# Kernel optimization log

Measured on AMD Instinct MI355X. Metric: run time of the kernel, lower is better.

## Reference

```python
import jax, jax.numpy as jnp
import numpy as np

JITTER = 0.1

def se_kernel(X, X2, length_scale):
    # K[i,j] = exp(-||x_i - x2_j||^2 / length_scale^2)   (no 1/2 factor, as in source)
    Xs = X / length_scale
    X2s = X2 / length_scale
    d2 = (jnp.sum(Xs * Xs, axis=1)[:, None]
          - 2.0 * Xs @ X2s.T
          + jnp.sum(X2s * X2s, axis=1)[None, :])
    return jnp.exp(-d2)

def kron(A, B):
    # kronecker(A, B) as in source: einsum 'ab,cd->acbd' then reshape
    return jnp.einsum('ab,cd->acbd', A, B).reshape(A.shape[0] * B.shape[0], A.shape[1] * B.shape[1])

def setup_inputs() -> dict:
    key = jax.random.key(0)
    ks = jax.random.split(key, 5)
    return {
        'space_coordinates': jax.random.normal(ks[0], (150, 3), dtype=jnp.float32),
        'time_coordinates': jax.random.normal(ks[1], (40, 1), dtype=jnp.float32),
        'stData': jax.random.normal(ks[2], (150, 40), dtype=jnp.float32),
        'test_space_coordinates': jax.random.normal(ks[3], (200, 3), dtype=jnp.float32),
        'test_time_coordinates': jax.random.normal(ks[4], (30, 1), dtype=jnp.float32),
        'log_latlong_length_scale': jnp.log(jnp.asarray(1.0, dtype=jnp.float32)),
        'log_elevation_length_scale': jnp.log(jnp.asarray(1.0, dtype=jnp.float32)),
        'log_time_length_scale': jnp.log(jnp.asarray(0.25, dtype=jnp.float32)),
        'log_noise_variance': jnp.log(jnp.asarray(0.1, dtype=jnp.float32)),
        'log_signal_variance': jnp.log(jnp.asarray(1.0, dtype=jnp.float32)),
    }

def reference(space_coordinates, time_coordinates, stData,
              test_space_coordinates, test_time_coordinates,
              log_latlong_length_scale, log_elevation_length_scale,
              log_time_length_scale, log_noise_variance, log_signal_variance):
    ll = jnp.exp(log_latlong_length_scale)
    le = jnp.exp(log_elevation_length_scale)
    lt = jnp.exp(log_time_length_scale)
    Ns = space_coordinates.shape[0]
    Nt = time_coordinates.shape[0]

    # ---- update(): build sigma_inverse and alpha via Kronecker eigendecomposition ----
    spatial_K = (se_kernel(space_coordinates[:, 0:2], space_coordinates[:, 0:2], ll)
                 * se_kernel(space_coordinates[:, 2:3], space_coordinates[:, 2:3], le)
                 + JITTER * jnp.eye(Ns, dtype=space_coordinates.dtype))
    temporal_K = (se_kernel(time_coordinates, time_coordinates, lt)
                  + JITTER * jnp.eye(Nt, dtype=time_coordinates.dtype))
    ws, Vs = jnp.linalg.eigh(spatial_K)
    wt, Vt = jnp.linalg.eigh(temporal_K)
    V = kron(Vt, Vs)                                   # [N, N], N = Nt*Ns
    w = jnp.einsum('a,b->ab', wt, ws).reshape(-1)      # eigenvalues of kron kernel
    inv = 1.0 / (w + jnp.exp(log_noise_variance))
    sigma_inverse = (V * inv[None, :]) @ V.T           # V diag(inv) V^T
    alpha = sigma_inverse @ stData.T.reshape(-1, 1)    # [N, 1]

    # ---- forward ----
    test_spatial = (se_kernel(test_space_coordinates[:, 0:2], space_coordinates[:, 0:2], ll)
                    * se_kernel(test_space_coordinates[:, 2:3], space_coordinates[:, 2:3], le))
    test_temporal = se_kernel(test_time_coordinates, time_coordinates, lt)
    Kst = kron(test_temporal, test_spatial)            # [M, N], M = Mt*Ms
    yPred = Kst @ alpha                                # [M, 1]
    # fused row-wise quadratic form: diag(Kst sigma_inverse Kst^T)
    yVar = jnp.exp(log_signal_variance) - jnp.sum((Kst @ sigma_inverse) * Kst, axis=1)
    Mt = test_time_coordinates.shape[0]
    Ms = test_space_coordinates.shape[0]
    yPred = yPred.reshape(Mt, Ms).T                    # [Ms, Mt]
    yVar = yVar.reshape(Mt, Ms).T                      # [Ms, Mt]
    return (yPred, yVar)
```

## Files before the change

kernel.cpp:

```cpp
#include <hip/hip_runtime.h>
#include <math.h>

#define NS 150
#define LDW 152
#define NPACK 11848
#define NT 40
#define MS 200
#define MT 30
#define N_SWEEPS 6
#define ROUNDS (N_SWEEPS*(NT-1))
#define JITTER 0.1f
#define NTHR 512

#define OFF_MP    0
#define OFF_PR    47392
#define OFF_INVS  52256
#define OFF_DVS   52288
#define OFF_SCS   52896
#define OFF_TSCS  54704
#define OFF_QV    57104
#define OFF_RV    57904
#define OFF_GV    58704
#define OFF_ACOL  59304
#define OFF_WTJ   59424
#define SMEM_BYTES 59440
#define OFF_A2    0
#define OFF_VTS   13120
#define OFF_PRM   20160
#define OFF_TCS   22720

__device__ __forceinline__ int rs_off(int r) {
    int g = r >> 2, rm = r & 3;
    return LDW * r - 8 * g * (g - 1) - 4 * rm * g;
}

__device__ __forceinline__ void jac_params(const float (*A)[NT+1], float4* dst,
                                           int i, int rr) {
    int i0 = i, i1 = NT - 1 - i;
    int p = (i0 == 0) ? 0 : ((i0 - 1 + rr) % (NT - 1)) + 1;
    int q = ((i1 - 1 + rr) % (NT - 1)) + 1;
    if (p > q) { int tsw = p; p = q; q = tsw; }
    float app = A[p][p], aqq = A[q][q], apq = A[p][q];
    float c, s;
    if (apq == 0.0f) { c = 1.0f; s = 0.0f; }
    else {
        float tau = (aqq - app) / (2.0f * apq);
        float tt = ((tau >= 0.0f) ? 1.0f : -1.0f) / (fabsf(tau) + sqrtf(1.0f + tau*tau));
        c = rsqrtf(1.0f + tt*tt);
        s = tt * c;
    }
    dst[i] = make_float4(c, s, __int_as_float(p), __int_as_float(q));
}

__global__ void __launch_bounds__(NTHR, 2) gp_block(
        const float* __restrict__ sc,  const float* __restrict__ tc,
        const float* __restrict__ st,  const float* __restrict__ tsc,
        const float* __restrict__ ttc,
        const float* __restrict__ lll, const float* __restrict__ lle,
        const float* __restrict__ llt, const float* __restrict__ lnv,
        const float* __restrict__ lsv, float* __restrict__ out) {
    __shared__ __align__(16) char smem[SMEM_BYTES];
    int j = blockIdx.x, tid = threadIdx.x;

    auto A2   = (float (*)[NT][NT+1])(smem + OFF_A2);
    auto Vts  = (float (*)[44])(smem + OFF_VTS);
    auto prm  = (float4 (*)[NT/2])(smem + OFF_PRM);
    float* tcs  = (float*)(smem + OFF_TCS);
    float* gv   = (float*)(smem + OFF_GV);
    float* Acol = (float*)(smem + OFF_ACOL);
    float* wtjs = (float*)(smem + OFF_WTJ);
    float* scs  = (float*)(smem + OFF_SCS);
    float* tscs = (float*)(smem + OFF_TSCS);

    float ilt2 = expf(-2.0f * llt[0]);
    if (tid < NT) tcs[tid] = tc[tid];
    for (int t = tid; t < NS*3; t += NTHR) scs[t] = sc[t];
    for (int t = tid; t < MS*3; t += NTHR) tscs[t] = tsc[t];
    __syncthreads();
    for (int idx = tid; idx < NT*NT; idx += NTHR) {
        int i = idx / NT, jj = idx - i*NT;
        float dt = tcs[i] - tcs[jj];
        float v = expf(-dt*dt*ilt2);
        if (i == jj) v += JITTER;
        A2[0][i][jj] = v;
    }
    for (int idx = tid; idx < NT*44; idx += NTHR) {
        int jr = idx / 44, k = idx - jr*44;
        Vts[jr][k] = (jr == k) ? 1.0f : 0.0f;
    }
    __syncthreads();
    int wave = tid >> 6, lane = tid & 63;
    for (int rd = 0; rd < ROUNDS; ++rd) {
        int cur = rd & 1, nxt = cur ^ 1;
        float4* wp = prm[wave];
        if (lane < NT/2) jac_params(A2[cur], wp, lane, rd % (NT - 1));
        __builtin_amdgcn_wave_barrier();
        for (int t = tid; t < 600; t += NTHR) {
            if (t < 400) {
                int bi = t / 20, bj = t - bi*20;
                float4 Pi = wp[bi], Pj = wp[bj];
                int pi = __float_as_int(Pi.z), qi = __float_as_int(Pi.w);
                int pj = __float_as_int(Pj.z), qj = __float_as_int(Pj.w);
                float ci = Pi.x, si = Pi.y, cj = Pj.x, sj = Pj.y;
                float a00 = A2[cur][pi][pj], a01 = A2[cur][pi][qj];
                float a10 = A2[cur][qi][pj], a11 = A2[cur][qi][qj];
                float b00 = ci*a00 - si*a10, b01 = ci*a01 - si*a11;
                float b10 = si*a00 + ci*a10, b11 = si*a01 + ci*a11;
                A2[nxt][pi][pj] = cj*b00 - sj*b01; A2[nxt][pi][qj] = sj*b00 + cj*b01;
                A2[nxt][qi][pj] = cj*b10 - sj*b11; A2[nxt][qi][qj] = sj*b10 + cj*b11;
            } else {
                int u2 = t - 400;
                int pr = u2 / 10, ch = (u2 - pr*10) << 2;
                float4 P = wp[pr];
                int pj = __float_as_int(P.z), qj = __float_as_int(P.w);
                float c = P.x, s = P.y;
                float4 vp = *(float4*)&Vts[pj][ch];
                float4 vq = *(float4*)&Vts[qj][ch];
                float4 np, nq;
                np.x = c*vp.x - s*vq.x; nq.x = s*vp.x + c*vq.x;
                np.y = c*vp.y - s*vq.y; nq.y = s*vp.y + c*vq.y;
                np.z = c*vp.z - s*vq.z; nq.z = s*vp.z + c*vq.z;
                np.w = c*vp.w - s*vq.w; nq.w = s*vp.w + c*vq.w;
                *(float4*)&Vts[pj][ch] = np;
                *(float4*)&Vts[qj][ch] = nq;
            }
        }
        __syncthreads();
    }
    const int fin = ROUNDS & 1;
    if (tid == 0) wtjs[0] = A2[fin][j][j];
    for (int s = tid; s < NS; s += NTHR) {
        const float4* va = (const float4*)&Vts[j][0];
        const float4* sa = (const float4*)&st[s*NT];
        float acc = 0.0f;
        #pragma unroll
        for (int c4 = 0; c4 < NT/4; ++c4) {
            float4 a = va[c4], b = sa[c4];
            acc += a.x*b.x + a.y*b.y + a.z*b.z + a.w*b.w;
        }
        gv[s] = acc;
    }
    if (tid < MT) {
        float ttv = ttc[tid];
        float acc = 0.0f;
        for (int t = 0; t < NT; ++t) {
            float dt = ttv - tcs[t];
            acc += expf(-dt*dt*ilt2) * Vts[j][t];
        }
        Acol[tid] = acc;
    }
    __syncthreads();

    float* Mp   = (float*)(smem + OFF_MP);
    auto   Pr   = (float (*)[LDW])(smem + OFF_PR);
    float* invs = (float*)(smem + OFF_INVS);
    float* dvs  = (float*)(smem + OFF_DVS);
    float* qv   = (float*)(smem + OFF_QV);
    float* Rv   = (float*)(smem + OFF_RV);
    float wtj = wtjs[0];
    float nv = expf(lnv[0]);
    float ill2 = expf(-2.0f * lll[0]);
    float ile2 = expf(-2.0f * lle[0]);
    for (int idx = tid; idx < NS*LDW; idx += NTHR) {
        int r = idx / LDW, c = idx - r*LDW;
        int rbase = r & ~3;
        if (c < rbase) continue;
        float v;
        if (c < NS) {
            float d0 = scs[r*3+0] - scs[c*3+0];
            float d1 = scs[r*3+1] - scs[c*3+1];
            float d2 = scs[r*3+2] - scs[c*3+2];
            v = wtj * expf(-((d0*d0 + d1*d1)*ill2 + d2*d2*ile2));
            if (c == r) v += wtj * JITTER + nv;
        } else if (c == NS) {
            v = gv[r];
        } else {
            v = 0.0f;
        }
        Mp[rs_off(r) + c - rbase] = v;
    }
    __syncthreads();
    for (int k0 = 0; k0 < NS - 1; k0 += 8) {
        int P = NS - k0; if (P > 8) P = 8;
        int W4 = (LDW - k0) >> 2;
        if (tid < W4) {
            int off[8];
            #pragma unroll
            for (int i = 0; i < 8; ++i)
                off[i] = (i < P) ? (rs_off(k0 + i) - ((i >= 4) ? 4 : 0)) : 0;
            float Bm[8][8];
            #pragma unroll
            for (int i = 0; i < 8; ++i) {
                #pragma unroll
                for (int c = 0; c < 8; ++c)
                    Bm[i][c] = (i < P && c >= i) ? Mp[off[i] + c]
                                                 : ((c == i) ? 1.0f : 0.0f);
            }
            float Lf[8][8]; float iv[8];
            #pragma unroll
            for (int k = 0; k < 8; ++k) {
                iv[k] = 1.0f / Bm[k][k];
                #pragma unroll
                for (int i = k + 1; i < 8; ++i) {
                    float l = Bm[k][i] * iv[k];
                    Lf[i][k] = l;
                    #pragma unroll
                    for (int c = i; c < 8; ++c) Bm[i][c] -= l * Bm[k][c];
                }
            }
            if (tid == 0) {
                #pragma unroll
                for (int i = 0; i < 8; ++i) invs[i] = iv[i];
            }
            int C = tid << 2;
            float4 m[8];
            #pragma unroll
            for (int i = 0; i < 8; ++i) {
                bool ok = (i < P) && (i < 4 || C >= 4);
                m[i] = ok ? *(float4*)&Mp[off[i] + C] : make_float4(0,0,0,0);
            }
            #pragma unroll
            for (int i = 1; i < 8; ++i) {
                #pragma unroll
                for (int k = 0; k < i; ++k) {
                    float l = Lf[i][k];
                    m[i].x -= l*m[k].x; m[i].y -= l*m[k].y;
                    m[i].z -= l*m[k].z; m[i].w -= l*m[k].w;
                }
            }
            #pragma unroll
            for (int i = 0; i < 8; ++i) *(float4*)&Pr[i][C] = m[i];
        }
        __syncthreads();
        for (int r = k0 + 1 + tid; r < NS; r += NTHR) {
            int rc = r - k0;
            float f[8];
            #pragma unroll
            for (int i = 0; i < 8; ++i)
                f[i] = (rc > i && i < P) ? Pr[i][rc] * invs[i] : 0.0f;
            int rbase = r & ~3;
            int ro = rs_off(r) - rbase;
            for (int C = rbase; C < LDW; C += 4) {
                int pc = C - k0;
                float4 v = *(float4*)&Mp[ro + C];
                #pragma unroll
                for (int i = 0; i < 8; ++i) {
                    float4 p = *(float4*)&Pr[i][pc];
                    v.x -= f[i]*p.x; v.y -= f[i]*p.y;
                    v.z -= f[i]*p.z; v.w -= f[i]*p.w;
                }
                *(float4*)&Mp[ro + C] = v;
            }
        }
        __syncthreads();
    }
    for (int r = tid; r < NS; r += NTHR)
        dvs[r] = rsqrtf(Mp[rs_off(r) + r - (r & ~3)]);
    __syncthreads();
    for (int idx = tid; idx < NS*LDW; idx += NTHR) {
        int r = idx / LDW, c = idx - r*LDW;
        int rbase = r & ~3;
        if (c < rbase) continue;
        int t = rs_off(r) + c - rbase;
        float dvr = dvs[r];
        if (c == r) Mp[t] = dvr;
        else if (c > r) Mp[t] *= dvr;
    }
    __syncthreads();
    if (tid < MS) {
        float tx = tscs[tid*3+0], ty = tscs[tid*3+1], tz = tscs[tid*3+2];
        float u[LDW];
        #pragma unroll
        for (int k = 0; k < NS; ++k) {
            float d0 = tx - scs[k*3+0];
            float d1 = ty - scs[k*3+1];
            float d2 = tz - scs[k*3+2];
            u[k] = expf(-((d0*d0 + d1*d1)*ill2 + d2*d2*ile2));
        }
        u[150] = 0.0f; u[151] = 0.0f;
        float qa = 0.0f, ra = 0.0f;
        #pragma unroll
        for (int k = 0; k < NS; ++k) {
            const int base = rs_off(k) - (k & ~3);
            float uk = u[k] * Mp[base + k];
            qa += uk * uk;
            ra += uk * Mp[base + 150];
            const int kp = k + 1;
            const int ka = (kp + 3) & ~3;
            #pragma unroll
            for (int t = kp; t < ((ka < NS) ? ka : NS); ++t)
                u[t] -= Mp[base + t] * uk;
            #pragma unroll
            for (int t = ka; t < NS; t += 4) {
                float4 w = *(const float4*)&Mp[base + t];
                u[t+0] -= w.x * uk; u[t+1] -= w.y * uk;
                u[t+2] -= w.z * uk; u[t+3] -= w.w * uk;
            }
        }
        qv[tid] = qa;
        Rv[tid] = ra;
    }
    __syncthreads();

    float sigv = expf(lsv[0]);
    for (int idx = tid; idx < MS*MT; idx += NTHR) {
        int is = idx / MT, it = idx - is*MT;
        float a = Acol[it];
        atomicAdd(&out[idx], a * Rv[is]);
        float c2 = -a * a * qv[is];
        if (j == 0) c2 += sigv;
        atomicAdd(&out[MS*MT + idx], c2);
    }
}

extern "C" void kernel_launch(void* const* d_in, const int* in_sizes, int n_in,
                              void* d_out, int out_size, void* d_ws, size_t ws_size,
                              hipStream_t stream) {
    const float* sc  = (const float*)d_in[0];
    const float* tc  = (const float*)d_in[1];
    const float* st  = (const float*)d_in[2];
    const float* tsc = (const float*)d_in[3];
    const float* ttc = (const float*)d_in[4];
    const float* lll = (const float*)d_in[5];
    const float* lle = (const float*)d_in[6];
    const float* llt = (const float*)d_in[7];
    const float* lnv = (const float*)d_in[8];
    const float* lsv = (const float*)d_in[9];
    float* out = (float*)d_out;

    hipMemsetAsync(out, 0, (size_t)out_size * sizeof(float), stream);
    hipLaunchKernelGGL(gp_block, dim3(NT), dim3(NTHR), 0, stream,
                       sc, tc, st, tsc, ttc, lll, lle, llt, lnv, lsv, out);
}
```

Measured before the change: 417.6 us.

## Replace atomic output accumulation with workspace plus reduction kernel; block triangular solve by 4

Each of the 40 blocks now writes its per-time-eigenvector coefficients, Rv and qv to a global workspace instead of atomically adding 12000 values into the output. A second small kernel reduces over the 40 blocks, which also removes the memset and the extra block-wide sync. The per-thread forward-substitution is restructured into 4-row blocks so each float4 row chunk updates u with four multipliers at once, cutting loop overhead and LDS read passes. The cost is an extra kernel launch, workspace traffic, and heavy register pressure from the fully unrolled macro code.

```diff
diff --git a/kernel.cpp b/kernel.cpp
--- a/kernel.cpp
+++ b/kernel.cpp
@@ -12,16 +12,17 @@
 #define JITTER 0.1f
 #define NTHR 512
 
+#define WS_AW 0
+#define WS_RV 1280
+#define WS_QV 11520
+
 #define OFF_MP    0
 #define OFF_PR    47392
 #define OFF_INVS  52256
 #define OFF_DVS   52288
 #define OFF_SCS   52896
 #define OFF_TSCS  54704
-#define OFF_QV    57104
-#define OFF_RV    57904
 #define OFF_GV    58704
-#define OFF_ACOL  59304
 #define OFF_WTJ   59424
 #define SMEM_BYTES 59440
 #define OFF_A2    0
@@ -32,6 +33,9 @@
 __device__ __forceinline__ int rs_off(int r) {
     int g = r >> 2, rm = r & 3;
     return LDW * r - 8 * g * (g - 1) - 4 * rm * g;
+}
+__device__ constexpr int rs_off_c(int r) {
+    return LDW * r - 8 * (r >> 2) * ((r >> 2) - 1) - 4 * (r & 3) * (r >> 2);
 }
 
 __device__ __forceinline__ void jac_params(const float (*A)[NT+1], float4* dst,
@@ -52,13 +56,53 @@
     dst[i] = make_float4(c, s, __int_as_float(p), __int_as_float(q));
 }
 
+#define ST4(K0) { \
+    constexpr int b0_ = rs_off_c((K0)+0) - ((K0) & ~3); \
+    constexpr int b1_ = rs_off_c((K0)+1) - ((K0) & ~3); \
+    constexpr int b2_ = rs_off_c((K0)+2) - ((K0) & ~3); \
+    constexpr int b3_ = rs_off_c((K0)+3) - ((K0) & ~3); \
+    float uk0_ = u[(K0)+0] * Mp[b0_ + (K0)+0]; \
+    qa += uk0_*uk0_;  ra += uk0_ * Mp[b0_ + 150]; \
+    u[(K0)+1] -= Mp[b0_ + (K0)+1] * uk0_; \
+    u[(K0)+2] -= Mp[b0_ + (K0)+2] * uk0_; \
+    u[(K0)+3] -= Mp[b0_ + (K0)+3] * uk0_; \
+    float uk1_ = u[(K0)+1] * Mp[b1_ + (K0)+1]; \
+    qa += uk1_*uk1_;  ra += uk1_ * Mp[b1_ + 150]; \
+    u[(K0)+2] -= Mp[b1_ + (K0)+2] * uk1_; \
+    u[(K0)+3] -= Mp[b1_ + (K0)+3] * uk1_; \
+    float uk2_ = u[(K0)+2] * Mp[b2_ + (K0)+2]; \
+    qa += uk2_*uk2_;  ra += uk2_ * Mp[b2_ + 150]; \
+    u[(K0)+3] -= Mp[b2_ + (K0)+3] * uk2_; \
+    float uk3_ = u[(K0)+3] * Mp[b3_ + (K0)+3]; \
+    qa += uk3_*uk3_;  ra += uk3_ * Mp[b3_ + 150]; \
+    _Pragma("unroll") \
+    for (int t_ = (K0)+4; t_ < NS; t_ += 4) { \
+        float4 w0_ = *(const float4*)&Mp[b0_ + t_]; \
+        float4 w1_ = *(const float4*)&Mp[b1_ + t_]; \
+        float4 w2_ = *(const float4*)&Mp[b2_ + t_]; \
+        float4 w3_ = *(const float4*)&Mp[b3_ + t_]; \
+        u[t_+0] -= w0_.x*uk0_ + w1_.x*uk1_ + w2_.x*uk2_ + w3_.x*uk3_; \
+        u[t_+1] -= w0_.y*uk0_ + w1_.y*uk1_ + w2_.y*uk2_ + w3_.y*uk3_; \
+        u[t_+2] -= w0_.z*uk0_ + w1_.z*uk1_ + w2_.z*uk2_ + w3_.z*uk3_; \
+        u[t_+3] -= w0_.w*uk0_ + w1_.w*uk1_ + w2_.w*uk2_ + w3_.w*uk3_; \
+    } \
+}
+
+#define UI(K) { \
+    float d0_ = tx - scs[(K)*3+0]; \
+    float d1_ = ty - scs[(K)*3+1]; \
+    float d2_ = tz - scs[(K)*3+2]; \
+    u[(K)] = expf(-((d0_*d0_ + d1_*d1_)*ill2 + d2_*d2_*ile2)); }
+#define UI10(K) UI((K)+0) UI((K)+1) UI((K)+2) UI((K)+3) UI((K)+4) \
+                UI((K)+5) UI((K)+6) UI((K)+7) UI((K)+8) UI((K)+9)
+
 __global__ void __launch_bounds__(NTHR, 2) gp_block(
         const float* __restrict__ sc,  const float* __restrict__ tc,
         const float* __restrict__ st,  const float* __restrict__ tsc,
         const float* __restrict__ ttc,
         const float* __restrict__ lll, const float* __restrict__ lle,
         const float* __restrict__ llt, const float* __restrict__ lnv,
-        const float* __restrict__ lsv, float* __restrict__ out) {
+        float* __restrict__ ws) {
     __shared__ __align__(16) char smem[SMEM_BYTES];
     int j = blockIdx.x, tid = threadIdx.x;
 
@@ -67,7 +111,6 @@
     auto prm  = (float4 (*)[NT/2])(smem + OFF_PRM);
     float* tcs  = (float*)(smem + OFF_TCS);
     float* gv   = (float*)(smem + OFF_GV);
-    float* Acol = (float*)(smem + OFF_ACOL);
     float* wtjs = (float*)(smem + OFF_WTJ);
     float* scs  = (float*)(smem + OFF_SCS);
     float* tscs = (float*)(smem + OFF_TSCS);
@@ -147,7 +190,7 @@
             float dt = ttv - tcs[t];
             acc += expf(-dt*dt*ilt2) * Vts[j][t];
         }
-        Acol[tid] = acc;
+        ws[WS_AW + j*32 + tid] = acc;
     }
     __syncthreads();
 
@@ -155,8 +198,6 @@
     auto   Pr   = (float (*)[LDW])(smem + OFF_PR);
     float* invs = (float*)(smem + OFF_INVS);
     float* dvs  = (float*)(smem + OFF_DVS);
-    float* qv   = (float*)(smem + OFF_QV);
-    float* Rv   = (float*)(smem + OFF_RV);
     float wtj = wtjs[0];
     float nv = expf(lnv[0]);
     float ill2 = expf(-2.0f * lll[0]);
@@ -269,48 +310,47 @@
     __syncthreads();
     if (tid < MS) {
         float tx = tscs[tid*3+0], ty = tscs[tid*3+1], tz = tscs[tid*3+2];
-        float u[LDW];
-        #pragma unroll
-        for (int k = 0; k < NS; ++k) {
-            float d0 = tx - scs[k*3+0];
-            float d1 = ty - scs[k*3+1];
-            float d2 = tz - scs[k*3+2];
-            u[k] = expf(-((d0*d0 + d1*d1)*ill2 + d2*d2*ile2));
-        }
+        float u[152];
+        UI10(0)  UI10(10) UI10(20) UI10(30) UI10(40)
+        UI10(50) UI10(60) UI10(70) UI10(80) UI10(90)
+        UI10(100) UI10(110) UI10(120) UI10(130) UI10(140)
         u[150] = 0.0f; u[151] = 0.0f;
         float qa = 0.0f, ra = 0.0f;
-        #pragma unroll
-        for (int k = 0; k < NS; ++k) {
-            const int base = rs_off(k) - (k & ~3);
-            float uk = u[k] * Mp[base + k];
-            qa += uk * uk;
-            ra += uk * Mp[base + 150];
-            const int kp = k + 1;
-            const int ka = (kp + 3) & ~3;
-            #pragma unroll
-            for (int t = kp; t < ((ka < NS) ? ka : NS); ++t)
-                u[t] -= Mp[base + t] * uk;
-            #pragma unroll
-            for (int t = ka; t < NS; t += 4) {
-                float4 w = *(const float4*)&Mp[base + t];
-                u[t+0] -= w.x * uk; u[t+1] -= w.y * uk;
-                u[t+2] -= w.z * uk; u[t+3] -= w.w * uk;
-            }
-        }
-        qv[tid] = qa;
-        Rv[tid] = ra;
-    }
-    __syncthreads();
-
-    float sigv = expf(lsv[0]);
-    for (int idx = tid; idx < MS*MT; idx += NTHR) {
-        int is = idx / MT, it = idx - is*MT;
-        float a = Acol[it];
-        atomicAdd(&out[idx], a * Rv[is]);
-        float c2 = -a * a * qv[is];
-        if (j == 0) c2 += sigv;
-        atomicAdd(&out[MS*MT + idx], c2);
-    }
+        ST4(0)   ST4(4)   ST4(8)   ST4(12)  ST4(16)  ST4(20)  ST4(24)
+        ST4(28)  ST4(32)  ST4(36)  ST4(40)  ST4(44)  ST4(48)  ST4(52)
+        ST4(56)  ST4(60)  ST4(64)  ST4(68)  ST4(72)  ST4(76)  ST4(80)
+        ST4(84)  ST4(88)  ST4(92)  ST4(96)  ST4(100) ST4(104) ST4(108)
+        ST4(112) ST4(116) ST4(120) ST4(124) ST4(128) ST4(132) ST4(136)
+        ST4(140) ST4(144)
+        {
+            constexpr int b8_ = rs_off_c(148) - 148;
+            constexpr int b9_ = rs_off_c(149) - 148;
+            float uk8_ = u[148] * Mp[b8_ + 148];
+            qa += uk8_*uk8_;  ra += uk8_ * Mp[b8_ + 150];
+            u[149] -= Mp[b8_ + 149] * uk8_;
+            float uk9_ = u[149] * Mp[b9_ + 149];
+            qa += uk9_*uk9_;  ra += uk9_ * Mp[b9_ + 150];
+        }
+        ws[WS_RV + j*256 + tid] = ra;
+        ws[WS_QV + j*256 + tid] = qa;
+    }
+}
+
+__global__ void __launch_bounds__(256) gp_reduce(
+        const float* __restrict__ ws, const float* __restrict__ lsv,
+        float* __restrict__ out) {
+    int idx = blockIdx.x * 256 + threadIdx.x;
+    if (idx >= MS*MT) return;
+    int is = idx / MT, it = idx - is*MT;
+    float p = 0.0f, q = 0.0f;
+    #pragma unroll
+    for (int jj = 0; jj < NT; ++jj) {
+        float a = ws[WS_AW + jj*32 + it];
+        p += a * ws[WS_RV + jj*256 + is];
+        q += a * a * ws[WS_QV + jj*256 + is];
+    }
+    out[idx] = p;
+    out[MS*MT + idx] = expf(lsv[0]) - q;
 }
 
 extern "C" void kernel_launch(void* const* d_in, const int* in_sizes, int n_in,
@@ -327,8 +367,10 @@
     const float* lnv = (const float*)d_in[8];
     const float* lsv = (const float*)d_in[9];
     float* out = (float*)d_out;
-
-    hipMemsetAsync(out, 0, (size_t)out_size * sizeof(float), stream);
+    float* ws  = (float*)d_ws;
+
     hipLaunchKernelGGL(gp_block, dim3(NT), dim3(NTHR), 0, stream,
-                       sc, tc, st, tsc, ttc, lll, lle, llt, lnv, lsv, out);
-}
+                       sc, tc, st, tsc, ttc, lll, lle, llt, lnv, ws);
+    hipLaunchKernelGGL(gp_reduce, dim3((MS*MT + 255)/256), dim3(256), 0, stream,
+                       ws, lsv, out);
+}
```

New measurement: 414.4 us. About the same (-0.8%).
